# Performance work log

Measured on AMD Instinct MI355X. Metric: run time of the kernel, lower is better.

## Reference

```python
import jax, jax.numpy as jnp
import numpy as np


def _gru_cell(x, h, wih, whh, bih, bhh):
    """PyTorch GRUCell semantics. x:[B,2] h:[B,2] wih/whh:[6,2] bih/bhh:[6]."""
    gi = x @ wih.T + bih  # [B,6]
    gh = h @ whh.T + bhh  # [B,6]
    i_r, i_z, i_n = jnp.split(gi, 3, axis=1)
    h_r, h_z, h_n = jnp.split(gh, 3, axis=1)
    r = jax.nn.sigmoid(i_r + h_r)
    z = jax.nn.sigmoid(i_z + h_z)
    n = jnp.tanh(i_n + r * h_n)
    return (1.0 - z) * n + z * h


def setup_inputs() -> dict:
    key = jax.random.key(0)
    ks = jax.random.split(key, 13)
    B = 1048576
    s = 0.5  # small init scale for stable gates
    return {
        "x": jax.random.normal(ks[0], (B, 19), dtype=jnp.float32),
        "up_wih": jax.random.normal(ks[1], (6, 2), dtype=jnp.float32) * s,
        "up_whh": jax.random.normal(ks[2], (6, 2), dtype=jnp.float32) * s,
        "up_bih": jax.random.normal(ks[3], (6,), dtype=jnp.float32) * s,
        "up_bhh": jax.random.normal(ks[4], (6,), dtype=jnp.float32) * s,
        "down_wih": jax.random.normal(ks[5], (6, 2), dtype=jnp.float32) * s,
        "down_whh": jax.random.normal(ks[6], (6, 2), dtype=jnp.float32) * s,
        "down_bih": jax.random.normal(ks[7], (6,), dtype=jnp.float32) * s,
        "down_bhh": jax.random.normal(ks[8], (6,), dtype=jnp.float32) * s,
        "obs_w": jax.random.normal(ks[9], (2, 7), dtype=jnp.float32) * s,
        "obs_b": jax.random.normal(ks[10], (2,), dtype=jnp.float32) * s,
        "out_w": jax.random.normal(ks[11], (1, 2), dtype=jnp.float32) * s,
        "out_b": jax.random.normal(ks[12], (1,), dtype=jnp.float32) * s,
    }


def reference(x, up_wih, up_whh, up_bih, up_bhh,
              down_wih, down_whh, down_bih, down_bhh,
              obs_w, obs_b, out_w, out_b):
    B = x.shape[0]
    obs = x[:, :5]                       # [B,5]
    j = x[:, 5:12]                       # [B,7]
    jd = x[:, 12:19]                     # [B,7]
    jcat = jnp.stack([j, jd], axis=-1)   # [B,7,2] per-joint (pos, vel)
    steps = jnp.swapaxes(jcat, 0, 1)     # [7,B,2]

    # up pass: scan r_up over the 7 joints, collecting hidden states
    h0 = jnp.zeros((B, 2), dtype=x.dtype)

    def up_step(h, inp):
        h_new = _gru_cell(inp, h, up_wih, up_whh, up_bih, up_bhh)
        return h_new, h_new

    h_last, h_up = jax.lax.scan(up_step, h0, steps)  # h_up: [7,B,2]

    # mix observation with final up hidden state
    h = jnp.concatenate([obs, h_last], axis=1) @ obs_w.T + obs_b  # [B,2]

    # down pass: scan r_down over stored up states, emitting actions
    def down_step(h, hu):
        h_new = _gru_cell(hu, h, down_wih, down_whh, down_bih, down_bhh)
        act = h_new @ out_w.T + out_b  # [B,1]
        return h_new, act

    _, acts = jax.lax.scan(down_step, h, h_up)  # [7,B,1]
    return jnp.swapaxes(acts, 0, 1)  # [B,7,1]
```

## Files before the change

### kernel.cpp

```cpp
#include <hip/hip_runtime.h>

#define TPB 256

__device__ __forceinline__ float fast_rcp(float x) { return __builtin_amdgcn_rcpf(x); }
__device__ __forceinline__ float sigm(float x) { return fast_rcp(1.0f + __expf(-x)); }
__device__ __forceinline__ float ftanh(float x) { return 1.0f - 2.0f * fast_rcp(__expf(2.0f * x) + 1.0f); }

__device__ __forceinline__ void gru_cell(const float* wih, const float* whh,
                                         const float* bih, const float* bhh,
                                         float x0, float x1, float& h0, float& h1) {
  float gi[6], gh[6];
#pragma unroll
  for (int g = 0; g < 6; ++g) {
    gi[g] = fmaf(wih[2 * g], x0, fmaf(wih[2 * g + 1], x1, bih[g]));
    gh[g] = fmaf(whh[2 * g], h0, fmaf(whh[2 * g + 1], h1, bhh[g]));
  }
  float r0 = sigm(gi[0] + gh[0]);
  float r1 = sigm(gi[1] + gh[1]);
  float z0 = sigm(gi[2] + gh[2]);
  float z1 = sigm(gi[3] + gh[3]);
  float n0 = ftanh(fmaf(r0, gh[4], gi[4]));
  float n1 = ftanh(fmaf(r1, gh[5], gi[5]));
  h0 = fmaf(z0, h0 - n0, n0);
  h1 = fmaf(z1, h1 - n1, n1);
}

__global__ __launch_bounds__(TPB) void rec_policy_kernel(
    const float* __restrict__ x,
    const float* __restrict__ up_wih, const float* __restrict__ up_whh,
    const float* __restrict__ up_bih, const float* __restrict__ up_bhh,
    const float* __restrict__ down_wih, const float* __restrict__ down_whh,
    const float* __restrict__ down_bih, const float* __restrict__ down_bhh,
    const float* __restrict__ obs_w, const float* __restrict__ obs_b,
    const float* __restrict__ out_w, const float* __restrict__ out_b,
    float* __restrict__ out, int B) {
  __shared__ float sx[TPB * 19];
  __shared__ float sout[TPB * 7];
  __shared__ float sw[91];

  const int tid = threadIdx.x;
  const int base = blockIdx.x * TPB;
  const int rows = min(TPB, B - base);

  if (tid < 91) {
    int i = tid;
    float v;
    if      (i < 12) v = up_wih[i];
    else if (i < 24) v = up_whh[i - 12];
    else if (i < 30) v = up_bih[i - 24];
    else if (i < 36) v = up_bhh[i - 30];
    else if (i < 48) v = down_wih[i - 36];
    else if (i < 60) v = down_whh[i - 48];
    else if (i < 66) v = down_bih[i - 60];
    else if (i < 72) v = down_bhh[i - 66];
    else if (i < 86) v = obs_w[i - 72];
    else if (i < 88) v = obs_b[i - 86];
    else if (i < 90) v = out_w[i - 88];
    else             v = out_b[0];
    sw[i] = v;
  }

  if (rows == TPB) {
    const float4* src = (const float4*)(x + (size_t)base * 19);
    float4* dst = (float4*)sx;
    for (int i = tid; i < TPB * 19 / 4; i += TPB) dst[i] = src[i];
  } else {
    for (int i = tid; i < rows * 19; i += TPB) sx[i] = x[(size_t)base * 19 + i];
  }
  __syncthreads();

  if (tid < rows) {
    const float* xr = sx + tid * 19;
    float hu[14];

    {
      float w[12], u[12], bi[6], bh[6];
#pragma unroll
      for (int i = 0; i < 12; ++i) { w[i] = sw[i]; u[i] = sw[12 + i]; }
#pragma unroll
      for (int i = 0; i < 6; ++i) { bi[i] = sw[24 + i]; bh[i] = sw[30 + i]; }
      float h0 = 0.f, h1 = 0.f;
#pragma unroll
      for (int t = 0; t < 7; ++t) {
        gru_cell(w, u, bi, bh, xr[5 + t], xr[12 + t], h0, h1);
        hu[2 * t] = h0;
        hu[2 * t + 1] = h1;
      }
    }

    float h0, h1;
    {
      float acc0 = sw[86], acc1 = sw[87];
#pragma unroll
      for (int k = 0; k < 5; ++k) {
        float c = xr[k];
        acc0 = fmaf(c, sw[72 + k], acc0);
        acc1 = fmaf(c, sw[79 + k], acc1);
      }
      acc0 = fmaf(hu[12], sw[77], fmaf(hu[13], sw[78], acc0));
      acc1 = fmaf(hu[12], sw[84], fmaf(hu[13], sw[85], acc1));
      h0 = acc0;
      h1 = acc1;
    }

    {
      float w[12], u[12], bi[6], bh[6];
#pragma unroll
      for (int i = 0; i < 12; ++i) { w[i] = sw[36 + i]; u[i] = sw[48 + i]; }
#pragma unroll
      for (int i = 0; i < 6; ++i) { bi[i] = sw[60 + i]; bh[i] = sw[66 + i]; }
      float ow0 = sw[88], ow1 = sw[89], ob = sw[90];
#pragma unroll
      for (int t = 0; t < 7; ++t) {
        gru_cell(w, u, bi, bh, hu[2 * t], hu[2 * t + 1], h0, h1);
        sout[tid * 7 + t] = fmaf(ow0, h0, fmaf(ow1, h1, ob));
      }
    }
  }
  __syncthreads();

  if (rows == TPB) {
    float4* dst = (float4*)(out + (size_t)base * 7);
    const float4* src = (const float4*)sout;
    for (int i = tid; i < TPB * 7 / 4; i += TPB) dst[i] = src[i];
  } else {
    for (int i = tid; i < rows * 7; i += TPB) out[(size_t)base * 7 + i] = sout[i];
  }
}

extern "C" void kernel_launch(void* const* d_in, const int* in_sizes, int n_in,
                              void* d_out, int out_size, void* d_ws, size_t ws_size,
                              hipStream_t stream) {
  const float* x        = (const float*)d_in[0];
  const float* up_wih   = (const float*)d_in[1];
  const float* up_whh   = (const float*)d_in[2];
  const float* up_bih   = (const float*)d_in[3];
  const float* up_bhh   = (const float*)d_in[4];
  const float* down_wih = (const float*)d_in[5];
  const float* down_whh = (const float*)d_in[6];
  const float* down_bih = (const float*)d_in[7];
  const float* down_bhh = (const float*)d_in[8];
  const float* obs_w    = (const float*)d_in[9];
  const float* obs_b    = (const float*)d_in[10];
  const float* out_w    = (const float*)d_in[11];
  const float* out_b    = (const float*)d_in[12];
  float* out = (float*)d_out;

  const int B = in_sizes[0] / 19;
  const int blocks = (B + TPB - 1) / TPB;
  rec_policy_kernel<<<blocks, TPB, 0, stream>>>(
      x, up_wih, up_whh, up_bih, up_bhh, down_wih, down_whh, down_bih, down_bhh,
      obs_w, obs_b, out_w, out_b, out, B);
}
```

Before: 154.5 us.

## Process two rows per thread with register-resident weights and exp2-based activations

Each thread now computes two rows per block (512 rows per 256-thread block), giving two independent recurrence chains for ILP and halving block count. Weights are loaded directly into registers via scalar loads instead of a shared-memory staging array, and the r/z biases are pre-summed. Activations use exp2 with pre-scaled constants, and the output staging reuses the input shared buffer. This raises register pressure and shared memory per block (launch bounds ask for 4 blocks/CU), which may reduce occupancy.

```diff
diff --git a/kernel.cpp b/kernel.cpp
--- a/kernel.cpp
+++ b/kernel.cpp
@@ -1,31 +1,91 @@
 #include <hip/hip_runtime.h>
 
 #define TPB 256
+#define RPB 512
 
-__device__ __forceinline__ float fast_rcp(float x) { return __builtin_amdgcn_rcpf(x); }
-__device__ __forceinline__ float sigm(float x) { return fast_rcp(1.0f + __expf(-x)); }
-__device__ __forceinline__ float ftanh(float x) { return 1.0f - 2.0f * fast_rcp(__expf(2.0f * x) + 1.0f); }
+__device__ __forceinline__ float ex2(float x) { return __builtin_amdgcn_exp2f(x); }
+__device__ __forceinline__ float frcp(float x) { return __builtin_amdgcn_rcpf(x); }
 
-__device__ __forceinline__ void gru_cell(const float* wih, const float* whh,
-                                         const float* bih, const float* bhh,
-                                         float x0, float x1, float& h0, float& h1) {
-  float gi[6], gh[6];
-#pragma unroll
-  for (int g = 0; g < 6; ++g) {
-    gi[g] = fmaf(wih[2 * g], x0, fmaf(wih[2 * g + 1], x1, bih[g]));
-    gh[g] = fmaf(whh[2 * g], h0, fmaf(whh[2 * g + 1], h1, bhh[g]));
-  }
-  float r0 = sigm(gi[0] + gh[0]);
-  float r1 = sigm(gi[1] + gh[1]);
-  float z0 = sigm(gi[2] + gh[2]);
-  float z1 = sigm(gi[3] + gh[3]);
-  float n0 = ftanh(fmaf(r0, gh[4], gi[4]));
-  float n1 = ftanh(fmaf(r1, gh[5], gi[5]));
+__device__ __forceinline__ float sigm(float x) {
+  return frcp(1.0f + ex2(-1.4426950408889634f * x));
+}
+__device__ __forceinline__ float ftanh(float x) {
+  return fmaf(-2.0f, frcp(ex2(2.8853900817779268f * x) + 1.0f), 1.0f);
+}
+
+struct GruW {
+  float w0, w1, w2, w3, w4, w5, w6, w7, w8, w9, w10, w11;
+  float u0, u1, u2, u3, u4, u5, u6, u7, u8, u9, u10, u11;
+  float br0, br1, bz0, bz1;
+  float bin0, bin1, bhn0, bhn1;
+};
+
+__device__ __forceinline__ GruW load_gru(const float* __restrict__ wih,
+                                         const float* __restrict__ whh,
+                                         const float* __restrict__ bih,
+                                         const float* __restrict__ bhh) {
+  GruW g;
+  g.w0 = wih[0];  g.w1 = wih[1];  g.w2 = wih[2];  g.w3 = wih[3];
+  g.w4 = wih[4];  g.w5 = wih[5];  g.w6 = wih[6];  g.w7 = wih[7];
+  g.w8 = wih[8];  g.w9 = wih[9];  g.w10 = wih[10]; g.w11 = wih[11];
+  g.u0 = whh[0];  g.u1 = whh[1];  g.u2 = whh[2];  g.u3 = whh[3];
+  g.u4 = whh[4];  g.u5 = whh[5];  g.u6 = whh[6];  g.u7 = whh[7];
+  g.u8 = whh[8];  g.u9 = whh[9];  g.u10 = whh[10]; g.u11 = whh[11];
+  g.br0 = bih[0] + bhh[0]; g.br1 = bih[1] + bhh[1];
+  g.bz0 = bih[2] + bhh[2]; g.bz1 = bih[3] + bhh[3];
+  g.bin0 = bih[4]; g.bin1 = bih[5];
+  g.bhn0 = bhh[4]; g.bhn1 = bhh[5];
+  return g;
+}
+
+__device__ __forceinline__ void cell(const GruW& g, float x0, float x1,
+                                     float& h0, float& h1) {
+  float r0 = sigm(fmaf(g.w0, x0, fmaf(g.w1, x1, fmaf(g.u0, h0, fmaf(g.u1, h1, g.br0)))));
+  float r1 = sigm(fmaf(g.w2, x0, fmaf(g.w3, x1, fmaf(g.u2, h0, fmaf(g.u3, h1, g.br1)))));
+  float z0 = sigm(fmaf(g.w4, x0, fmaf(g.w5, x1, fmaf(g.u4, h0, fmaf(g.u5, h1, g.bz0)))));
+  float z1 = sigm(fmaf(g.w6, x0, fmaf(g.w7, x1, fmaf(g.u6, h0, fmaf(g.u7, h1, g.bz1)))));
+  float gin0 = fmaf(g.w8, x0, fmaf(g.w9, x1, g.bin0));
+  float gin1 = fmaf(g.w10, x0, fmaf(g.w11, x1, g.bin1));
+  float ghn0 = fmaf(g.u8, h0, fmaf(g.u9, h1, g.bhn0));
+  float ghn1 = fmaf(g.u10, h0, fmaf(g.u11, h1, g.bhn1));
+  float n0 = ftanh(fmaf(r0, ghn0, gin0));
+  float n1 = ftanh(fmaf(r1, ghn1, gin1));
   h0 = fmaf(z0, h0 - n0, n0);
   h1 = fmaf(z1, h1 - n1, n1);
 }
 
-__global__ __launch_bounds__(TPB) void rec_policy_kernel(
+__device__ __forceinline__ void row_compute(
+    const float* __restrict__ xr, const GruW& up, const GruW& dn,
+    float ow0, float ow1, float ow2, float ow3, float ow4, float ow5, float ow6,
+    float ow7, float ow8, float ow9, float ow10, float ow11, float ow12, float ow13,
+    float ob0, float ob1, float vw0, float vw1, float vb,
+    float& o0, float& o1, float& o2, float& o3, float& o4, float& o5, float& o6) {
+  float h0 = 0.f, h1 = 0.f;
+  float hu0, hu1, hu2, hu3, hu4, hu5, hu6, hu7, hu8, hu9, hu10, hu11, hu12, hu13;
+  cell(up, xr[5],  xr[12], h0, h1); hu0 = h0;  hu1 = h1;
+  cell(up, xr[6],  xr[13], h0, h1); hu2 = h0;  hu3 = h1;
+  cell(up, xr[7],  xr[14], h0, h1); hu4 = h0;  hu5 = h1;
+  cell(up, xr[8],  xr[15], h0, h1); hu6 = h0;  hu7 = h1;
+  cell(up, xr[9],  xr[16], h0, h1); hu8 = h0;  hu9 = h1;
+  cell(up, xr[10], xr[17], h0, h1); hu10 = h0; hu11 = h1;
+  cell(up, xr[11], xr[18], h0, h1); hu12 = h0; hu13 = h1;
+
+  float a0 = fmaf(xr[0], ow0, fmaf(xr[1], ow1, fmaf(xr[2], ow2, fmaf(xr[3], ow3,
+             fmaf(xr[4], ow4, fmaf(hu12, ow5, fmaf(hu13, ow6, ob0)))))));
+  float a1 = fmaf(xr[0], ow7, fmaf(xr[1], ow8, fmaf(xr[2], ow9, fmaf(xr[3], ow10,
+             fmaf(xr[4], ow11, fmaf(hu12, ow12, fmaf(hu13, ow13, ob1)))))));
+  h0 = a0; h1 = a1;
+
+  cell(dn, hu0,  hu1,  h0, h1); o0 = fmaf(vw0, h0, fmaf(vw1, h1, vb));
+  cell(dn, hu2,  hu3,  h0, h1); o1 = fmaf(vw0, h0, fmaf(vw1, h1, vb));
+  cell(dn, hu4,  hu5,  h0, h1); o2 = fmaf(vw0, h0, fmaf(vw1, h1, vb));
+  cell(dn, hu6,  hu7,  h0, h1); o3 = fmaf(vw0, h0, fmaf(vw1, h1, vb));
+  cell(dn, hu8,  hu9,  h0, h1); o4 = fmaf(vw0, h0, fmaf(vw1, h1, vb));
+  cell(dn, hu10, hu11, h0, h1); o5 = fmaf(vw0, h0, fmaf(vw1, h1, vb));
+  cell(dn, hu12, hu13, h0, h1); o6 = fmaf(vw0, h0, fmaf(vw1, h1, vb));
+}
+
+__global__ __launch_bounds__(TPB, 4) void rec_policy_kernel(
     const float* __restrict__ x,
     const float* __restrict__ up_wih, const float* __restrict__ up_whh,
     const float* __restrict__ up_bih, const float* __restrict__ up_bhh,
@@ -34,97 +94,65 @@
     const float* __restrict__ obs_w, const float* __restrict__ obs_b,
     const float* __restrict__ out_w, const float* __restrict__ out_b,
     float* __restrict__ out, int B) {
-  __shared__ float sx[TPB * 19];
-  __shared__ float sout[TPB * 7];
-  __shared__ float sw[91];
+  __shared__ __align__(16) float sx[RPB * 19];
 
   const int tid = threadIdx.x;
-  const int base = blockIdx.x * TPB;
-  const int rows = min(TPB, B - base);
+  const long base = (long)blockIdx.x * RPB;
+  const int rows = min((long)RPB, (long)B - base);
 
-  if (tid < 91) {
-    int i = tid;
-    float v;
-    if      (i < 12) v = up_wih[i];
-    else if (i < 24) v = up_whh[i - 12];
-    else if (i < 30) v = up_bih[i - 24];
-    else if (i < 36) v = up_bhh[i - 30];
-    else if (i < 48) v = down_wih[i - 36];
-    else if (i < 60) v = down_whh[i - 48];
-    else if (i < 66) v = down_bih[i - 60];
-    else if (i < 72) v = down_bhh[i - 66];
-    else if (i < 86) v = obs_w[i - 72];
-    else if (i < 88) v = obs_b[i - 86];
-    else if (i < 90) v = out_w[i - 88];
-    else             v = out_b[0];
-    sw[i] = v;
-  }
+  const GruW up = load_gru(up_wih, up_whh, up_bih, up_bhh);
+  const GruW dn = load_gru(down_wih, down_whh, down_bih, down_bhh);
+  const float ow0 = obs_w[0], ow1 = obs_w[1], ow2 = obs_w[2], ow3 = obs_w[3],
+              ow4 = obs_w[4], ow5 = obs_w[5], ow6 = obs_w[6], ow7 = obs_w[7],
+              ow8 = obs_w[8], ow9 = obs_w[9], ow10 = obs_w[10], ow11 = obs_w[11],
+              ow12 = obs_w[12], ow13 = obs_w[13];
+  const float ob0 = obs_b[0], ob1 = obs_b[1];
+  const float vw0 = out_w[0], vw1 = out_w[1], vb = out_b[0];
 
-  if (rows == TPB) {
-    const float4* src = (const float4*)(x + (size_t)base * 19);
-    float4* dst = (float4*)sx;
-    for (int i = tid; i < TPB * 19 / 4; i += TPB) dst[i] = src[i];
+  if (rows == RPB) {
+    {
+      const float4* src = (const float4*)(x + base * 19);
+      float4* dst = (float4*)sx;
+      for (int i = tid; i < RPB * 19 / 4; i += TPB) dst[i] = src[i];
+    }
+    __syncthreads();
+
+    const float* xa = sx + tid * 19;
+    const float* xb = sx + (tid + TPB) * 19;
+    float ao0, ao1, ao2, ao3, ao4, ao5, ao6;
+    float bo0, bo1, bo2, bo3, bo4, bo5, bo6;
+    row_compute(xa, up, dn, ow0, ow1, ow2, ow3, ow4, ow5, ow6, ow7, ow8, ow9,
+                ow10, ow11, ow12, ow13, ob0, ob1, vw0, vw1, vb,
+                ao0, ao1, ao2, ao3, ao4, ao5, ao6);
+    row_compute(xb, up, dn, ow0, ow1, ow2, ow3, ow4, ow5, ow6, ow7, ow8, ow9,
+                ow10, ow11, ow12, ow13, ob0, ob1, vw0, vw1, vb,
+                bo0, bo1, bo2, bo3, bo4, bo5, bo6);
+
+    __syncthreads();
+    float* soa = sx + tid * 7;
+    soa[0] = ao0; soa[1] = ao1; soa[2] = ao2; soa[3] = ao3;
+    soa[4] = ao4; soa[5] = ao5; soa[6] = ao6;
+    float* sob = sx + (tid + TPB) * 7;
+    sob[0] = bo0; sob[1] = bo1; sob[2] = bo2; sob[3] = bo3;
+    sob[4] = bo4; sob[5] = bo5; sob[6] = bo6;
+    __syncthreads();
+
+    float4* dst = (float4*)(out + base * 7);
+    const float4* s4 = (const float4*)sx;
+    for (int i = tid; i < RPB * 7 / 4; i += TPB) dst[i] = s4[i];
   } else {
-    for (int i = tid; i < rows * 19; i += TPB) sx[i] = x[(size_t)base * 19 + i];
-  }
-  __syncthreads();
-
-  if (tid < rows) {
-    const float* xr = sx + tid * 19;
-    float hu[14];
-
-    {
-      float w[12], u[12], bi[6], bh[6];
-#pragma unroll
-      for (int i = 0; i < 12; ++i) { w[i] = sw[i]; u[i] = sw[12 + i]; }
-#pragma unroll
-      for (int i = 0; i < 6; ++i) { bi[i] = sw[24 + i]; bh[i] = sw[30 + i]; }
-      float h0 = 0.f, h1 = 0.f;
-#pragma unroll
-      for (int t = 0; t < 7; ++t) {
-        gru_cell(w, u, bi, bh, xr[5 + t], xr[12 + t], h0, h1);
-        hu[2 * t] = h0;
-        hu[2 * t + 1] = h1;
-      }
+    for (int i = tid; i < rows * 19; i += TPB) sx[i] = x[base * 19 + i];
+    __syncthreads();
+    for (int r = tid; r < rows; r += TPB) {
+      const float* xr = sx + r * 19;
+      float o0, o1, o2, o3, o4, o5, o6;
+      row_compute(xr, up, dn, ow0, ow1, ow2, ow3, ow4, ow5, ow6, ow7, ow8, ow9,
+                  ow10, ow11, ow12, ow13, ob0, ob1, vw0, vw1, vb,
+                  o0, o1, o2, o3, o4, o5, o6);
+      float* po = out + (base + r) * 7;
+      po[0] = o0; po[1] = o1; po[2] = o2; po[3] = o3;
+      po[4] = o4; po[5] = o5; po[6] = o6;
     }
-
-    float h0, h1;
-    {
-      float acc0 = sw[86], acc1 = sw[87];
-#pragma unroll
-      for (int k = 0; k < 5; ++k) {
-        float c = xr[k];
-        acc0 = fmaf(c, sw[72 + k], acc0);
-        acc1 = fmaf(c, sw[79 + k], acc1);
-      }
-      acc0 = fmaf(hu[12], sw[77], fmaf(hu[13], sw[78], acc0));
-      acc1 = fmaf(hu[12], sw[84], fmaf(hu[13], sw[85], acc1));
-      h0 = acc0;
-      h1 = acc1;
-    }
-
-    {
-      float w[12], u[12], bi[6], bh[6];
-#pragma unroll
-      for (int i = 0; i < 12; ++i) { w[i] = sw[36 + i]; u[i] = sw[48 + i]; }
-#pragma unroll
-      for (int i = 0; i < 6; ++i) { bi[i] = sw[60 + i]; bh[i] = sw[66 + i]; }
-      float ow0 = sw[88], ow1 = sw[89], ob = sw[90];
-#pragma unroll
-      for (int t = 0; t < 7; ++t) {
-        gru_cell(w, u, bi, bh, hu[2 * t], hu[2 * t + 1], h0, h1);
-        sout[tid * 7 + t] = fmaf(ow0, h0, fmaf(ow1, h1, ob));
-      }
-    }
-  }
-  __syncthreads();
-
-  if (rows == TPB) {
-    float4* dst = (float4*)(out + (size_t)base * 7);
-    const float4* src = (const float4*)sout;
-    for (int i = tid; i < TPB * 7 / 4; i += TPB) dst[i] = src[i];
-  } else {
-    for (int i = tid; i < rows * 7; i += TPB) out[(size_t)base * 7 + i] = sout[i];
   }
 }
 
@@ -147,7 +175,7 @@
   float* out = (float*)d_out;
 
   const int B = in_sizes[0] / 19;
-  const int blocks = (B + TPB - 1) / TPB;
+  const int blocks = (B + RPB - 1) / RPB;
   rec_policy_kernel<<<blocks, TPB, 0, stream>>>(
       x, up_wih, up_whh, up_bih, up_bhh, down_wih, down_whh, down_bih, down_bhh,
       obs_w, obs_b, out_w, out_b, out, B);
```

Measured after the change: 156.1 us. No clear change (+1.1%).
